# Optimization experiments

Hardware: AMD Instinct MI355X
Metric: run time of the kernel (lower is better)

The kernel has to match this reference:

```python
import jax, jax.numpy as jnp
import numpy as np

B, H, S, D, HID, A = 16384, 15, 32, 256, 256, 6


def setup_inputs() -> dict:
    key = jax.random.key(0)
    ks = iter(jax.random.split(key, 32))
    rn = lambda shape, scale=1.0: jax.random.normal(next(ks), shape, dtype=jnp.float32) * scale
    w = 0.05  # small weight init scale
    return {
        "stoch_state": rn((B, S)),
        "gru_state": rn((B, D)),
        "act_noise": rn((H, B, A)),
        "stoch_noise": rn((H, B, S)),
        "W_a0": rn((HID, S + D), w), "b_a0": jnp.zeros((HID,), jnp.float32),
        "W_a1": rn((HID, HID), w),   "b_a1": jnp.zeros((HID,), jnp.float32),
        "W_am": rn((A, HID), w),     "b_am": jnp.zeros((A,), jnp.float32),
        "W_as": rn((A, HID), w),     "b_as": jnp.zeros((A,), jnp.float32),
        "W_img": rn((HID, S + A), w), "b_img": jnp.zeros((HID,), jnp.float32),
        "W_ih": rn((3 * D, HID), w), "b_ih": jnp.zeros((3 * D,), jnp.float32),
        "W_hh": rn((3 * D, D), w),   "b_hh": jnp.zeros((3 * D,), jnp.float32),
        "W_p0": rn((HID, D), w),     "b_p0": jnp.zeros((HID,), jnp.float32),
        "W_pm": rn((S, HID), w),     "b_pm": jnp.zeros((S,), jnp.float32),
        "W_ps": rn((S, HID), w),     "b_ps": jnp.zeros((S,), jnp.float32),
    }


def _lin(x, W, b):
    return x @ W.T + b


def _gru_cell(x, h, W_ih, b_ih, W_hh, b_hh):
    # torch.nn.GRUCell gate layout: [reset, update, new]
    gi = _lin(x, W_ih, b_ih)
    gh = _lin(h, W_hh, b_hh)
    ir, iz, inn = jnp.split(gi, 3, axis=-1)
    hr, hz, hn = jnp.split(gh, 3, axis=-1)
    r = jax.nn.sigmoid(ir + hr)
    z = jax.nn.sigmoid(iz + hz)
    n = jnp.tanh(inn + r * hn)
    return (1.0 - z) * n + z * h


def dream(stoch_state, gru_state, act_noise, stoch_noise,
          W_a0, b_a0, W_a1, b_a1, W_am, b_am, W_as, b_as,
          W_img, b_img, W_ih, b_ih, W_hh, b_hh,
          W_p0, b_p0, W_pm, b_pm, W_ps, b_ps):
    def step(carry, noise):
        stoch, gru = carry
        an, sn = noise
        state = jnp.concatenate([stoch, gru], axis=-1)
        # action model on detached state (as in original dream())
        sd = jax.lax.stop_gradient(state)
        ah = jax.nn.elu(_lin(sd, W_a0, b_a0))
        ah = jax.nn.elu(_lin(ah, W_a1, b_a1))
        a_mean = _lin(ah, W_am, b_am)
        a_std = jax.nn.softplus(_lin(ah, W_as, b_as))
        action = a_mean + a_std * an  # rsample
        # img1 MLP
        x = jax.nn.elu(_lin(jnp.concatenate([stoch, action], axis=-1), W_img, b_img))
        # GRU cell
        gru = _gru_cell(x, gru, W_ih, b_ih, W_hh, b_hh)
        # prior model rsample
        ph = jax.nn.elu(_lin(gru, W_p0, b_p0))
        p_mean = _lin(ph, W_pm, b_pm)
        p_std = jax.nn.softplus(_lin(ph, W_ps, b_ps))
        stoch = p_mean + p_std * sn
        out = jnp.concatenate([stoch, gru], axis=-1)  # [B, S+D]
        return (stoch, gru), out

    _, states = jax.lax.scan(step, (stoch_state, gru_state), (act_noise, stoch_noise))
    return states  # [H, B, S+D]


def reference(stoch_state, gru_state, act_noise, stoch_noise,
              W_a0, b_a0, W_a1, b_a1, W_am, b_am, W_as, b_as,
              W_img, b_img, W_ih, b_ih, W_hh, b_hh,
              W_p0, b_p0, W_pm, b_pm, W_ps, b_ps):
    return dream(stoch_state, gru_state, act_noise, stoch_noise,
                 W_a0, b_a0, W_a1, b_a1, W_am, b_am, W_as, b_as,
                 W_img, b_img, W_ih, b_ih, W_hh, b_hh,
                 W_p0, b_p0, W_pm, b_pm, W_ps, b_ps)
```

## Files before the change

### kernel.cpp

```cpp
#include <hip/hip_runtime.h>
#include <hip/hip_bf16.h>

#define MFMA_BF16 __builtin_amdgcn_mfma_f32_16x16x32_bf16

typedef __attribute__((ext_vector_type(8))) short short8;
typedef __attribute__((ext_vector_type(4))) float f32x4;

#define NB 16384
#define NH 15
#define NS 32
#define ND 256
#define NHID 256
#define NA 6

#define OFF_A0   0
#define OFF_A1   73728
#define OFF_AMS  139264
#define OFF_IMG  143360
#define OFF_IH   159744
#define OFF_HH   356352
#define OFF_P0   552960
#define OFF_PMS  618496
#define W_TOTAL  634880

__device__ __forceinline__ short f2b(float v){ __hip_bfloat16 b = __float2bfloat16(v); return __builtin_bit_cast(short, b); }
__device__ __forceinline__ float b2f(short s){ return __bfloat162float(__builtin_bit_cast(__hip_bfloat16, s)); }
__device__ __forceinline__ float sigm(float x){ return 1.f/(1.f + __expf(-x)); }
__device__ __forceinline__ float softp(float x){ return fmaxf(x,0.f) + log1pf(__expf(-fabsf(x))); }
__device__ __forceinline__ float eluf(float x){ return x>0.f ? x : (__expf(x)-1.f); }

__device__ __forceinline__ void decode_frag(int m, int KB, int& row, int& k){
  int tidx = m >> 9, w = m & 511;
  int lane = w >> 3, e = w & 7;
  int t = tidx / KB, kb = tidx - t*KB;
  row = t*16 + (lane & 15);
  k   = kb*32 + ((lane >> 4) << 3) + e;
}

__global__ void pack_w(const float* __restrict__ a0, const float* __restrict__ a1,
                       const float* __restrict__ am, const float* __restrict__ as,
                       const float* __restrict__ img, const float* __restrict__ ih,
                       const float* __restrict__ hh, const float* __restrict__ p0,
                       const float* __restrict__ pm, const float* __restrict__ ps,
                       short* __restrict__ ws){
  int i = blockIdx.x*256 + threadIdx.x;
  if (i >= W_TOTAL) return;
  int row, k; float v;
  if (i < OFF_A1){        decode_frag(i - OFF_A0, 9, row, k);  v = a0[row*288 + k]; }
  else if (i < OFF_AMS){  decode_frag(i - OFF_A1, 8, row, k);  v = a1[row*256 + k]; }
  else if (i < OFF_IMG){  decode_frag(i - OFF_AMS, 8, row, k);
                          v = row<6 ? am[row*256+k] : (row<12 ? as[(row-6)*256+k] : 0.f); }
  else if (i < OFF_IH){   decode_frag(i - OFF_IMG, 2, row, k);
                          v = k<38 ? img[row*38 + k] : 0.f; }
  else if (i < OFF_HH){   decode_frag(i - OFF_IH, 8, row, k);  v = ih[row*256 + k]; }
  else if (i < OFF_P0){   decode_frag(i - OFF_HH, 8, row, k);  v = hh[row*256 + k]; }
  else if (i < OFF_PMS){  decode_frag(i - OFF_P0, 8, row, k);  v = p0[row*256 + k]; }
  else {                  decode_frag(i - OFF_PMS, 8, row, k);
                          v = row<32 ? pm[row*256+k] : ps[(row-32)*256+k]; }
  ws[i] = f2b(v);
}

template<int KB, bool ELU>
__device__ __forceinline__ void dense_slice(const short* __restrict__ Ab, int astr,
                                            const short* __restrict__ W,
                                            const float* __restrict__ bias,
                                            short* __restrict__ Ob,
                                            int tbase, int n0, int lane, int lk){
  f32x4 acc[2][2] = {};
  const short* ap = Ab + (lane & 15)*astr + lk*8;
  const int astep = 16*astr;
  const short* wl = W + lane*8;
  #pragma unroll
  for (int kb=0; kb<KB; ++kb){
    short8 a0 = *(const short8*)(ap + kb*32);
    short8 a1 = *(const short8*)(ap + astep + kb*32);
    #pragma unroll
    for (int j=0; j<2; ++j){
      short8 b = *(const short8*)(wl + ((tbase + j)*KB + kb)*512);
      acc[0][j] = MFMA_BF16(a0, b, acc[0][j], 0, 0, 0);
      acc[1][j] = MFMA_BF16(a1, b, acc[1][j], 0, 0, 0);
    }
  }
  #pragma unroll
  for (int mt=0; mt<2; ++mt){
    #pragma unroll
    for (int j=0; j<2; ++j){
      int n = n0 + j*16;
      float bs = bias[n];
      #pragma unroll
      for (int i=0; i<4; ++i){
        int row = mt*16 + lk*4 + i;
        float v = acc[mt][j][i] + bs;
        Ob[row*264 + n] = f2b(ELU ? eluf(v) : v);
      }
    }
  }
}

__global__ __launch_bounds__(256) void dream_kernel(
    const float* __restrict__ stoch0, const float* __restrict__ gru0,
    const float* __restrict__ anoise, const float* __restrict__ snoise,
    const short* __restrict__ ws,
    const float* __restrict__ b_a0, const float* __restrict__ b_a1,
    const float* __restrict__ b_am, const float* __restrict__ b_as,
    const float* __restrict__ b_img, const float* __restrict__ b_ih,
    const float* __restrict__ b_hh, const float* __restrict__ b_p0,
    const float* __restrict__ b_pm, const float* __restrict__ b_ps,
    float* __restrict__ out)
{
  __shared__ short bufA[32*264];
  __shared__ short bufB[32*264];
  __shared__ short bufC[32*264];
  __shared__ short simg[32*72];

  const int tid   = threadIdx.x;
  const int wid   = tid >> 6;
  const int lane  = tid & 63;
  const int lrow  = lane & 15;
  const int lk    = lane >> 4;
  const int r0    = blockIdx.x * 32;
  const int tb0   = wid * 4;
  const int n00   = wid * 64 + lrow;
  const int tb1   = wid * 4 + 2;
  const int n01   = wid * 64 + 32 + lrow;

  for (int idx = tid; idx < 32*256; idx += 256){
    int r = idx >> 8, c = idx & 255;
    bufA[r*264 + c] = f2b(gru0[(size_t)(r0+r)*256 + c]);
  }
  for (int idx = tid; idx < 32*32; idx += 256){
    int r = idx >> 5, c = idx & 31;
    simg[r*72 + c]      = f2b(stoch0[(size_t)(r0+r)*32 + c]);
    simg[r*72 + 32 + c] = 0;
  }
  __syncthreads();

  short* G = bufA;
  short* X = bufB;
  short* Y = bufC;

  for (int h = 0; h < NH; ++h){
    #pragma unroll 1
    for (int half=0; half<2; ++half){
      const int tbase = half ? tb1 : tb0;
      const int n0    = half ? n01 : n00;
      f32x4 acc[2][2] = {};
      const short* ai = simg + lrow*72  + lk*8;
      const short* ag = G    + lrow*264 + lk*8;
      const short* wl = ws + OFF_A0 + lane*8;
      #pragma unroll
      for (int kb=0; kb<9; ++kb){
        short8 a0 = (kb==0) ? *(const short8*)ai : *(const short8*)(ag + (kb-1)*32);
        short8 a1 = (kb==0) ? *(const short8*)(ai + 16*72) : *(const short8*)(ag + 16*264 + (kb-1)*32);
        #pragma unroll
        for (int j=0; j<2; ++j){
          short8 b = *(const short8*)(wl + ((tbase + j)*9 + kb)*512);
          acc[0][j] = MFMA_BF16(a0, b, acc[0][j], 0, 0, 0);
          acc[1][j] = MFMA_BF16(a1, b, acc[1][j], 0, 0, 0);
        }
      }
      #pragma unroll
      for (int mt=0; mt<2; ++mt)
        #pragma unroll
        for (int j=0; j<2; ++j){
          int n = n0 + j*16;
          float bs = b_a0[n];
          #pragma unroll
          for (int i=0; i<4; ++i){
            int row = mt*16 + lk*4 + i;
            X[row*264 + n] = f2b(eluf(acc[mt][j][i] + bs));
          }
        }
    }
    __syncthreads();

    dense_slice<8,true>(X, 264, ws + OFF_A1, b_a1, Y, tb0, n00, lane, lk);
    dense_slice<8,true>(X, 264, ws + OFF_A1, b_a1, Y, tb1, n01, lane, lk);
    __syncthreads();

    if (wid < 2){
      const int mt = wid;
      f32x4 acc = {};
      const short* ap = Y + (mt*16+lrow)*264 + lk*8;
      const short* wl = ws + OFF_AMS + lane*8;
      #pragma unroll
      for (int kb=0; kb<8; ++kb){
        short8 a = *(const short8*)(ap + kb*32);
        short8 b = *(const short8*)(wl + kb*512);
        acc = MFMA_BF16(a, b, acc, 0, 0, 0);
      }
      float bs = (lrow<6) ? b_am[lrow] : (lrow<12 ? b_as[lrow-6] : 0.f);
      #pragma unroll
      for (int i=0; i<4; ++i){
        float raw = acc[i] + bs;
        float sp  = softp(raw);
        float spn = __shfl(sp, (lane & 48) | ((lrow + 6) & 15));
        if (lrow < 6){
          int row = mt*16 + lk*4 + i;
          size_t grow = r0 + row;
          float an = __builtin_nontemporal_load(&anoise[((size_t)h*NB + grow)*NA + lrow]);
          simg[row*72 + 32 + lrow] = f2b(raw + spn * an);
        }
      }
    }
    __syncthreads();

    dense_slice<2,true>(simg, 72, ws + OFF_IMG, b_img, X, tb0, n00, lane, lk);
    dense_slice<2,true>(simg, 72, ws + OFF_IMG, b_img, X, tb1, n01, lane, lk);
    __syncthreads();

    {
      const short* wl_ih = ws + OFF_IH + lane*8;
      const short* wl_hh = ws + OFF_HH + lane*8;
      #pragma unroll 1
      for (int mtl=0; mtl<2; ++mtl){
        const int rbase = mtl*16;
        const short* xp = X + (rbase+lrow)*264 + lk*8;
        const short* gp = G + (rbase+lrow)*264 + lk*8;
        #pragma unroll 1
        for (int jj=0; jj<4; ++jj){
          f32x4 aR = {}, aZ = {}, aI = {}, aH = {};
          const int tr = wid*4 + jj;
          #pragma unroll
          for (int kb=0; kb<8; ++kb){
            short8 br = *(const short8*)(wl_ih + ((tr     )*8 + kb)*512);
            short8 bz = *(const short8*)(wl_ih + ((tr + 16)*8 + kb)*512);
            short8 bn = *(const short8*)(wl_ih + ((tr + 32)*8 + kb)*512);
            short8 cr = *(const short8*)(wl_hh + ((tr     )*8 + kb)*512);
            short8 cz = *(const short8*)(wl_hh + ((tr + 16)*8 + kb)*512);
            short8 ch = *(const short8*)(wl_hh + ((tr + 32)*8 + kb)*512);
            short8 ax = *(const short8*)(xp + kb*32);
            short8 ag = *(const short8*)(gp + kb*32);
            aR = MFMA_BF16(ax, br, aR, 0, 0, 0);
            aZ = MFMA_BF16(ax, bz, aZ, 0, 0, 0);
            aI = MFMA_BF16(ax, bn, aI, 0, 0, 0);
            aR = MFMA_BF16(ag, cr, aR, 0, 0, 0);
            aZ = MFMA_BF16(ag, cz, aZ, 0, 0, 0);
            aH = MFMA_BF16(ag, ch, aH, 0, 0, 0);
          }
          int c = wid*64 + jj*16 + lrow;
          float bir = b_ih[c]       + b_hh[c];
          float biz = b_ih[256 + c] + b_hh[256 + c];
          float bin = b_ih[512 + c];
          float bhn = b_hh[512 + c];
          #pragma unroll
          for (int i=0; i<4; ++i){
            int row = rbase + lk*4 + i;
            float hold = b2f(G[row*264 + c]);
            float r = sigm(aR[i] + bir);
            float z = sigm(aZ[i] + biz);
            float n = tanhf(aI[i] + bin + r*(aH[i] + bhn));
            float hnew = (1.f - z)*n + z*hold;
            Y[row*264 + c] = f2b(hnew);
            __builtin_nontemporal_store(hnew, &out[((size_t)h*NB + (size_t)(r0+row))*288 + 32 + c]);
          }
        }
      }
    }
    __syncthreads();

    dense_slice<8,true>(Y, 264, ws + OFF_P0, b_p0, X, tb0, n00, lane, lk);
    dense_slice<8,true>(Y, 264, ws + OFF_P0, b_p0, X, tb1, n01, lane, lk);
    __syncthreads();

    {
      const int mt = wid & 1;
      const int jp = wid >> 1;
      f32x4 accM = {}, accS = {};
      const short* ap = X + (mt*16+lrow)*264 + lk*8;
      const short* wl = ws + OFF_PMS + lane*8;
      #pragma unroll
      for (int kb=0; kb<8; ++kb){
        short8 a  = *(const short8*)(ap + kb*32);
        short8 bm = *(const short8*)(wl + ((jp    )*8 + kb)*512);
        short8 bs = *(const short8*)(wl + ((jp + 2)*8 + kb)*512);
        accM = MFMA_BF16(a, bm, accM, 0, 0, 0);
        accS = MFMA_BF16(a, bs, accS, 0, 0, 0);
      }
      int sc = jp*16 + lrow;
      float bm = b_pm[sc], bp = b_ps[sc];
      #pragma unroll
      for (int i=0; i<4; ++i){
        int row = mt*16 + lk*4 + i;
        size_t grow = r0 + row;
        float m  = accM[i] + bm;
        float sp = softp(accS[i] + bp);
        float sn = __builtin_nontemporal_load(&snoise[((size_t)h*NB + grow)*NS + sc]);
        float st = m + sp*sn;
        simg[row*72 + sc] = f2b(st);
        __builtin_nontemporal_store(st, &out[((size_t)h*NB + grow)*288 + sc]);
      }
    }
    __syncthreads();

    short* t = G; G = Y; Y = X; X = t;
  }
}

extern "C" void kernel_launch(void* const* d_in, const int* in_sizes, int n_in,
                              void* d_out, int out_size, void* d_ws, size_t ws_size,
                              hipStream_t stream){
  const float* stoch0 = (const float*)d_in[0];
  const float* gru0   = (const float*)d_in[1];
  const float* anoise = (const float*)d_in[2];
  const float* snoise = (const float*)d_in[3];
  const float* Wa0 = (const float*)d_in[4];   const float* ba0 = (const float*)d_in[5];
  const float* Wa1 = (const float*)d_in[6];   const float* ba1 = (const float*)d_in[7];
  const float* Wam = (const float*)d_in[8];   const float* bam = (const float*)d_in[9];
  const float* Was = (const float*)d_in[10];  const float* bas = (const float*)d_in[11];
  const float* Wimg= (const float*)d_in[12];  const float* bimg= (const float*)d_in[13];
  const float* Wih = (const float*)d_in[14];  const float* bih = (const float*)d_in[15];
  const float* Whh = (const float*)d_in[16];  const float* bhh = (const float*)d_in[17];
  const float* Wp0 = (const float*)d_in[18];  const float* bp0 = (const float*)d_in[19];
  const float* Wpm = (const float*)d_in[20];  const float* bpm = (const float*)d_in[21];
  const float* Wps = (const float*)d_in[22];  const float* bps = (const float*)d_in[23];
  short* ws  = (short*)d_ws;
  float* out = (float*)d_out;

  pack_w<<<(W_TOTAL + 255)/256, 256, 0, stream>>>(Wa0, Wa1, Wam, Was, Wimg, Wih, Whh, Wp0, Wpm, Wps, ws);
  dream_kernel<<<NB/32, 256, 0, stream>>>(stoch0, gru0, anoise, snoise, ws,
                                          ba0, ba1, bam, bas, bimg, bih, bhh, bp0, bpm, bps, out);
}
```

Baseline: 1.226 ms.

## Halve rows per block to 16 for more blocks and higher occupancy

Each block now processes 16 batch rows instead of 32, so 1024 blocks launch instead of 512 and LDS per block is halved. The launch bound asks for 4 blocks per CU. The aim is more waves in flight per CU to hide latency. In exchange, every weight fragment read from global or L2 now feeds only one MFMA row tile instead of two, which doubles weight traffic per row, and some small heads leave more waves idle.

Result: slower. 2.187 ms (+78.4%).

```diff
diff --git a/kernel.cpp b/kernel.cpp
--- a/kernel.cpp
+++ b/kernel.cpp
@@ -61,43 +61,37 @@
 }
 
 template<int KB, bool ELU>
-__device__ __forceinline__ void dense_slice(const short* __restrict__ Ab, int astr,
-                                            const short* __restrict__ W,
-                                            const float* __restrict__ bias,
-                                            short* __restrict__ Ob,
-                                            int tbase, int n0, int lane, int lk){
-  f32x4 acc[2][2] = {};
+__device__ __forceinline__ void dense16(const short* __restrict__ Ab, int astr,
+                                        const short* __restrict__ W,
+                                        const float* __restrict__ bias,
+                                        short* __restrict__ Ob,
+                                        int tbase, int n0, int lane, int lk){
+  f32x4 acc[2] = {};
   const short* ap = Ab + (lane & 15)*astr + lk*8;
-  const int astep = 16*astr;
   const short* wl = W + lane*8;
   #pragma unroll
   for (int kb=0; kb<KB; ++kb){
-    short8 a0 = *(const short8*)(ap + kb*32);
-    short8 a1 = *(const short8*)(ap + astep + kb*32);
+    short8 a = *(const short8*)(ap + kb*32);
     #pragma unroll
     for (int j=0; j<2; ++j){
       short8 b = *(const short8*)(wl + ((tbase + j)*KB + kb)*512);
-      acc[0][j] = MFMA_BF16(a0, b, acc[0][j], 0, 0, 0);
-      acc[1][j] = MFMA_BF16(a1, b, acc[1][j], 0, 0, 0);
+      acc[j] = MFMA_BF16(a, b, acc[j], 0, 0, 0);
     }
   }
   #pragma unroll
-  for (int mt=0; mt<2; ++mt){
+  for (int j=0; j<2; ++j){
+    int n = n0 + j*16;
+    float bs = bias[n];
     #pragma unroll
-    for (int j=0; j<2; ++j){
-      int n = n0 + j*16;
-      float bs = bias[n];
-      #pragma unroll
-      for (int i=0; i<4; ++i){
-        int row = mt*16 + lk*4 + i;
-        float v = acc[mt][j][i] + bs;
-        Ob[row*264 + n] = f2b(ELU ? eluf(v) : v);
-      }
-    }
-  }
-}
-
-__global__ __launch_bounds__(256) void dream_kernel(
+    for (int i=0; i<4; ++i){
+      int row = lk*4 + i;
+      float v = acc[j][i] + bs;
+      Ob[row*264 + n] = f2b(ELU ? eluf(v) : v);
+    }
+  }
+}
+
+__global__ __launch_bounds__(256, 4) void dream_kernel(
     const float* __restrict__ stoch0, const float* __restrict__ gru0,
     const float* __restrict__ anoise, const float* __restrict__ snoise,
     const short* __restrict__ ws,
@@ -108,27 +102,27 @@
     const float* __restrict__ b_pm, const float* __restrict__ b_ps,
     float* __restrict__ out)
 {
-  __shared__ short bufA[32*264];
-  __shared__ short bufB[32*264];
-  __shared__ short bufC[32*264];
-  __shared__ short simg[32*72];
+  __shared__ short bufA[16*264];
+  __shared__ short bufB[16*264];
+  __shared__ short bufC[16*264];
+  __shared__ short simg[16*72];
 
   const int tid   = threadIdx.x;
   const int wid   = tid >> 6;
   const int lane  = tid & 63;
   const int lrow  = lane & 15;
   const int lk    = lane >> 4;
-  const int r0    = blockIdx.x * 32;
+  const int r0    = blockIdx.x * 16;
   const int tb0   = wid * 4;
   const int n00   = wid * 64 + lrow;
   const int tb1   = wid * 4 + 2;
   const int n01   = wid * 64 + 32 + lrow;
 
-  for (int idx = tid; idx < 32*256; idx += 256){
+  for (int idx = tid; idx < 16*256; idx += 256){
     int r = idx >> 8, c = idx & 255;
     bufA[r*264 + c] = f2b(gru0[(size_t)(r0+r)*256 + c]);
   }
-  for (int idx = tid; idx < 32*32; idx += 256){
+  for (int idx = tid; idx < 16*32; idx += 256){
     int r = idx >> 5, c = idx & 31;
     simg[r*72 + c]      = f2b(stoch0[(size_t)(r0+r)*32 + c]);
     simg[r*72 + 32 + c] = 0;
@@ -144,44 +138,39 @@
     for (int half=0; half<2; ++half){
       const int tbase = half ? tb1 : tb0;
       const int n0    = half ? n01 : n00;
-      f32x4 acc[2][2] = {};
+      f32x4 acc[2] = {};
       const short* ai = simg + lrow*72  + lk*8;
       const short* ag = G    + lrow*264 + lk*8;
       const short* wl = ws + OFF_A0 + lane*8;
       #pragma unroll
       for (int kb=0; kb<9; ++kb){
-        short8 a0 = (kb==0) ? *(const short8*)ai : *(const short8*)(ag + (kb-1)*32);
-        short8 a1 = (kb==0) ? *(const short8*)(ai + 16*72) : *(const short8*)(ag + 16*264 + (kb-1)*32);
+        short8 a = (kb==0) ? *(const short8*)ai : *(const short8*)(ag + (kb-1)*32);
         #pragma unroll
         for (int j=0; j<2; ++j){
           short8 b = *(const short8*)(wl + ((tbase + j)*9 + kb)*512);
-          acc[0][j] = MFMA_BF16(a0, b, acc[0][j], 0, 0, 0);
-          acc[1][j] = MFMA_BF16(a1, b, acc[1][j], 0, 0, 0);
-        }
-      }
-      #pragma unroll
-      for (int mt=0; mt<2; ++mt)
+          acc[j] = MFMA_BF16(a, b, acc[j], 0, 0, 0);
+        }
+      }
+      #pragma unroll
+      for (int j=0; j<2; ++j){
+        int n = n0 + j*16;
+        float bs = b_a0[n];
         #pragma unroll
-        for (int j=0; j<2; ++j){
-          int n = n0 + j*16;
-          float bs = b_a0[n];
-          #pragma unroll
-          for (int i=0; i<4; ++i){
-            int row = mt*16 + lk*4 + i;
-            X[row*264 + n] = f2b(eluf(acc[mt][j][i] + bs));
-          }
-        }
-    }
-    __syncthreads();
-
-    dense_slice<8,true>(X, 264, ws + OFF_A1, b_a1, Y, tb0, n00, lane, lk);
-    dense_slice<8,true>(X, 264, ws + OFF_A1, b_a1, Y, tb1, n01, lane, lk);
-    __syncthreads();
-
-    if (wid < 2){
-      const int mt = wid;
+        for (int i=0; i<4; ++i){
+          int row = lk*4 + i;
+          X[row*264 + n] = f2b(eluf(acc[j][i] + bs));
+        }
+      }
+    }
+    __syncthreads();
+
+    dense16<8,true>(X, 264, ws + OFF_A1, b_a1, Y, tb0, n00, lane, lk);
+    dense16<8,true>(X, 264, ws + OFF_A1, b_a1, Y, tb1, n01, lane, lk);
+    __syncthreads();
+
+    if (wid == 0){
       f32x4 acc = {};
-      const short* ap = Y + (mt*16+lrow)*264 + lk*8;
+      const short* ap = Y + lrow*264 + lk*8;
       const short* wl = ws + OFF_AMS + lane*8;
       #pragma unroll
       for (int kb=0; kb<8; ++kb){
@@ -196,7 +185,7 @@
         float sp  = softp(raw);
         float spn = __shfl(sp, (lane & 48) | ((lrow + 6) & 15));
         if (lrow < 6){
-          int row = mt*16 + lk*4 + i;
+          int row = lk*4 + i;
           size_t grow = r0 + row;
           float an = __builtin_nontemporal_load(&anoise[((size_t)h*NB + grow)*NA + lrow]);
           simg[row*72 + 32 + lrow] = f2b(raw + spn * an);
@@ -205,69 +194,64 @@
     }
     __syncthreads();
 
-    dense_slice<2,true>(simg, 72, ws + OFF_IMG, b_img, X, tb0, n00, lane, lk);
-    dense_slice<2,true>(simg, 72, ws + OFF_IMG, b_img, X, tb1, n01, lane, lk);
+    dense16<2,true>(simg, 72, ws + OFF_IMG, b_img, X, tb0, n00, lane, lk);
+    dense16<2,true>(simg, 72, ws + OFF_IMG, b_img, X, tb1, n01, lane, lk);
     __syncthreads();
 
     {
       const short* wl_ih = ws + OFF_IH + lane*8;
       const short* wl_hh = ws + OFF_HH + lane*8;
+      const short* xp = X + lrow*264 + lk*8;
+      const short* gp = G + lrow*264 + lk*8;
       #pragma unroll 1
-      for (int mtl=0; mtl<2; ++mtl){
-        const int rbase = mtl*16;
-        const short* xp = X + (rbase+lrow)*264 + lk*8;
-        const short* gp = G + (rbase+lrow)*264 + lk*8;
-        #pragma unroll 1
-        for (int jj=0; jj<4; ++jj){
-          f32x4 aR = {}, aZ = {}, aI = {}, aH = {};
-          const int tr = wid*4 + jj;
-          #pragma unroll
-          for (int kb=0; kb<8; ++kb){
-            short8 br = *(const short8*)(wl_ih + ((tr     )*8 + kb)*512);
-            short8 bz = *(const short8*)(wl_ih + ((tr + 16)*8 + kb)*512);
-            short8 bn = *(const short8*)(wl_ih + ((tr + 32)*8 + kb)*512);
-            short8 cr = *(const short8*)(wl_hh + ((tr     )*8 + kb)*512);
-            short8 cz = *(const short8*)(wl_hh + ((tr + 16)*8 + kb)*512);
-            short8 ch = *(const short8*)(wl_hh + ((tr + 32)*8 + kb)*512);
-            short8 ax = *(const short8*)(xp + kb*32);
-            short8 ag = *(const short8*)(gp + kb*32);
-            aR = MFMA_BF16(ax, br, aR, 0, 0, 0);
-            aZ = MFMA_BF16(ax, bz, aZ, 0, 0, 0);
-            aI = MFMA_BF16(ax, bn, aI, 0, 0, 0);
-            aR = MFMA_BF16(ag, cr, aR, 0, 0, 0);
-            aZ = MFMA_BF16(ag, cz, aZ, 0, 0, 0);
-            aH = MFMA_BF16(ag, ch, aH, 0, 0, 0);
-          }
-          int c = wid*64 + jj*16 + lrow;
-          float bir = b_ih[c]       + b_hh[c];
-          float biz = b_ih[256 + c] + b_hh[256 + c];
-          float bin = b_ih[512 + c];
-          float bhn = b_hh[512 + c];
-          #pragma unroll
-          for (int i=0; i<4; ++i){
-            int row = rbase + lk*4 + i;
-            float hold = b2f(G[row*264 + c]);
-            float r = sigm(aR[i] + bir);
-            float z = sigm(aZ[i] + biz);
-            float n = tanhf(aI[i] + bin + r*(aH[i] + bhn));
-            float hnew = (1.f - z)*n + z*hold;
-            Y[row*264 + c] = f2b(hnew);
-            __builtin_nontemporal_store(hnew, &out[((size_t)h*NB + (size_t)(r0+row))*288 + 32 + c]);
-          }
-        }
-      }
-    }
-    __syncthreads();
-
-    dense_slice<8,true>(Y, 264, ws + OFF_P0, b_p0, X, tb0, n00, lane, lk);
-    dense_slice<8,true>(Y, 264, ws + OFF_P0, b_p0, X, tb1, n01, lane, lk);
-    __syncthreads();
-
-    {
-      const int mt = wid & 1;
-      const int jp = wid >> 1;
+      for (int jj=0; jj<4; ++jj){
+        f32x4 aR = {}, aZ = {}, aI = {}, aH = {};
+        const int tr = wid*4 + jj;
+        #pragma unroll
+        for (int kb=0; kb<8; ++kb){
+          short8 br = *(const short8*)(wl_ih + ((tr     )*8 + kb)*512);
+          short8 bz = *(const short8*)(wl_ih + ((tr + 16)*8 + kb)*512);
+          short8 bn = *(const short8*)(wl_ih + ((tr + 32)*8 + kb)*512);
+          short8 cr = *(const short8*)(wl_hh + ((tr     )*8 + kb)*512);
+          short8 cz = *(const short8*)(wl_hh + ((tr + 16)*8 + kb)*512);
+          short8 ch = *(const short8*)(wl_hh + ((tr + 32)*8 + kb)*512);
+          short8 ax = *(const short8*)(xp + kb*32);
+          short8 ag = *(const short8*)(gp + kb*32);
+          aR = MFMA_BF16(ax, br, aR, 0, 0, 0);
+          aZ = MFMA_BF16(ax, bz, aZ, 0, 0, 0);
+          aI = MFMA_BF16(ax, bn, aI, 0, 0, 0);
+          aR = MFMA_BF16(ag, cr, aR, 0, 0, 0);
+          aZ = MFMA_BF16(ag, cz, aZ, 0, 0, 0);
+          aH = MFMA_BF16(ag, ch, aH, 0, 0, 0);
+        }
+        int c = wid*64 + jj*16 + lrow;
+        float bir = b_ih[c]       + b_hh[c];
+        float biz = b_ih[256 + c] + b_hh[256 + c];
+        float bin = b_ih[512 + c];
+        float bhn = b_hh[512 + c];
+        #pragma unroll
+        for (int i=0; i<4; ++i){
+          int row = lk*4 + i;
+          float hold = b2f(G[row*264 + c]);
+          float r = sigm(aR[i] + bir);
+          float z = sigm(aZ[i] + biz);
+          float n = tanhf(aI[i] + bin + r*(aH[i] + bhn));
+          float hnew = (1.f - z)*n + z*hold;
+          Y[row*264 + c] = f2b(hnew);
+          __builtin_nontemporal_store(hnew, &out[((size_t)h*NB + (size_t)(r0+row))*288 + 32 + c]);
+        }
+      }
+    }
+    __syncthreads();
+
+    dense16<8,true>(Y, 264, ws + OFF_P0, b_p0, X, tb0, n00, lane, lk);
+    dense16<8,true>(Y, 264, ws + OFF_P0, b_p0, X, tb1, n01, lane, lk);
+    __syncthreads();
+
+    if (wid < 2){
+      const int jp = wid;
       f32x4 accM = {}, accS = {};
-      const short* ap = X + (mt*16+lrow)*264 + lk*8;
+      const short* ap = X + lrow*264 + lk*8;
       const short* wl = ws + OFF_PMS + lane*8;
       #pragma unroll
       for (int kb=0; kb<8; ++kb){
@@ -281,7 +265,7 @@
       float bm = b_pm[sc], bp = b_ps[sc];
       #pragma unroll
       for (int i=0; i<4; ++i){
-        int row = mt*16 + lk*4 + i;
+        int row = lk*4 + i;
         size_t grow = r0 + row;
         float m  = accM[i] + bm;
         float sp = softp(accS[i] + bp);
@@ -318,6 +302,6 @@
   float* out = (float*)d_out;
 
   pack_w<<<(W_TOTAL + 255)/256, 256, 0, stream>>>(Wa0, Wa1, Wam, Was, Wimg, Wih, Whh, Wp0, Wpm, Wps, ws);
-  dream_kernel<<<NB/32, 256, 0, stream>>>(stoch0, gru0, anoise, snoise, ws,
+  dream_kernel<<<NB/16, 256, 0, stream>>>(stoch0, gru0, anoise, snoise, ws,
                                           ba0, ba1, bam, bas, bimg, bih, bhh, bp0, bpm, bps, out);
 }
```
